# Kernel optimization log

Measured on AMD Instinct MI355X. Metric: run time of the kernel, lower is better.

## Reference

```python
import jax, jax.numpy as jnp
import numpy as np

N, E, D, H, O = 50000, 800000, 128, 256, 64
BN_EPS = 1e-5


def setup_inputs() -> dict:
    key = jax.random.key(0)
    ks = jax.random.split(key, 12)
    x_indices = jnp.arange(N, dtype=jnp.int64) if jax.config.jax_enable_x64 else jnp.arange(N, dtype=jnp.int32)
    ei = jax.random.randint(ks[0], (2, E), 0, N, dtype=jnp.int32)
    s = lambda k, shape, fan: jax.random.normal(k, shape, dtype=jnp.float32) * (1.0 / np.sqrt(fan))
    return {
        "x_indices": x_indices,
        "ei": ei,
        "emb": jax.random.normal(ks[1], (N, D), dtype=jnp.float32),
        "W1": s(ks[2], (D, H), D), "b1": jnp.zeros((H,), jnp.float32),
        "g1": jnp.ones((H,), jnp.float32), "be1": jnp.zeros((H,), jnp.float32),
        "W2": s(ks[3], (H, H), H), "b2": jnp.zeros((H,), jnp.float32),
        "g2": jnp.ones((H,), jnp.float32), "be2": jnp.zeros((H,), jnp.float32),
        "W3": s(ks[4], (H, O), H), "b3": jnp.zeros((O,), jnp.float32),
    }


def reference(x_indices, ei, emb, W1, b1, g1, be1, W2, b2, g2, be2, W3, b3):
    n = emb.shape[0]
    # GCN normalization with self-loops (PyG GCNConv default):
    loop = jnp.arange(n, dtype=ei.dtype)
    row = jnp.concatenate([ei[0], loop])  # source
    col = jnp.concatenate([ei[1], loop])  # target (aggregation index)
    deg = jax.ops.segment_sum(jnp.ones_like(col, dtype=emb.dtype), col, num_segments=n)
    dinv = jnp.where(deg > 0, 1.0 / jnp.sqrt(jnp.maximum(deg, 1.0)), 0.0)
    norm = dinv[row] * dinv[col]  # [E+N]

    def conv(x, W, b):
        xl = x @ W                                   # [N, d_out]
        msg = xl[row] * norm[:, None]                # gather + scale
        return jax.ops.segment_sum(msg, col, num_segments=n) + b  # scatter-add

    def bn(x, g, be):  # batch-stat BatchNorm1d (training-mode stats)
        m = jnp.mean(x, axis=0)
        v = jnp.var(x, axis=0)
        return (x - m) * (g / jnp.sqrt(v + BN_EPS)) + be

    x = emb[x_indices]
    x = jax.nn.relu(bn(conv(x, W1, b1), g1, be1))
    x = jax.nn.relu(bn(conv(x, W2, b2), g2, be2))
    return conv(x, W3, b3)
```

## Files before the change

kernel.cpp:

```cpp
#include <hip/hip_runtime.h>
#include <hip/hip_bf16.h>

#define Dk 128
#define Hk 256
#define Ok 64
#define BN_EPS 1e-5f

typedef __attribute__((ext_vector_type(8))) short short8;
typedef __attribute__((ext_vector_type(4))) float f32x4;

static __device__ __forceinline__ float bf2f(ushort u) {
    union { uint32_t i; float f; } c; c.i = ((uint32_t)u) << 16; return c.f;
}
static __device__ __forceinline__ ushort f2bf(float f) {
    union { float f; uint32_t u; } c; c.f = f;
    return (ushort)((c.u + 0x7fffu + ((c.u >> 16) & 1u)) >> 16);
}

template<int V> __device__ __forceinline__ void loadv(ushort* d, const ushort* s);
template<> __device__ __forceinline__ void loadv<1>(ushort* d, const ushort* s) { d[0] = *s; }
template<> __device__ __forceinline__ void loadv<2>(ushort* d, const ushort* s) { *(ushort2*)d = *(const ushort2*)s; }
template<> __device__ __forceinline__ void loadv<4>(ushort* d, const ushort* s) { *(ushort4*)d = *(const ushort4*)s; }
template<int V> __device__ __forceinline__ void storev(ushort* d, const ushort* s);
template<> __device__ __forceinline__ void storev<1>(ushort* d, const ushort* s) { *d = s[0]; }
template<> __device__ __forceinline__ void storev<2>(ushort* d, const ushort* s) { *(ushort2*)d = *(const ushort2*)s; }
template<> __device__ __forceinline__ void storev<4>(ushort* d, const ushort* s) { *(ushort4*)d = *(const ushort4*)s; }


__global__ void count_kernel(const int* __restrict__ col, int* __restrict__ cnt, int E) {
    int e = blockIdx.x * blockDim.x + threadIdx.x;
    if (e < E) atomicAdd(&cnt[col[e]], 1);
}

__global__ void dinv_bsum_kernel(const int* __restrict__ cnt, float* __restrict__ dinv,
                                 int* __restrict__ fillc, int* __restrict__ bsum, int n) {
    __shared__ int sm[256];
    int i = blockIdx.x * 256 + threadIdx.x;
    int c = (i < n) ? cnt[i] : 0;
    if (i < n) { dinv[i] = rsqrtf((float)c + 1.0f); fillc[i] = 0; }
    sm[threadIdx.x] = c;
    __syncthreads();
    for (int s = 128; s; s >>= 1) {
        if (threadIdx.x < s) sm[threadIdx.x] += sm[threadIdx.x + s];
        __syncthreads();
    }
    if (!threadIdx.x) bsum[blockIdx.x] = sm[0];
}

__global__ void scan_base_kernel(int* __restrict__ bsum, int nb) {
    __shared__ int sm[256];
    int t = threadIdx.x;
    int carry = 0;
    for (int base = 0; base < nb; base += 256) {
        int i = base + t;
        int v = (i < nb) ? bsum[i] : 0;
        sm[t] = v;
        __syncthreads();
        for (int s = 1; s < 256; s <<= 1) {
            int add = (t >= s) ? sm[t - s] : 0;
            __syncthreads();
            sm[t] += add;
            __syncthreads();
        }
        if (i < nb) bsum[i] = carry + sm[t] - v;
        int tot = sm[255];
        __syncthreads();
        carry += tot;
    }
}

__global__ void scan_final_kernel(const int* __restrict__ cnt, const int* __restrict__ bbase,
                                  int* __restrict__ offv, int n) {
    __shared__ int sm[256];
    int t = threadIdx.x, i = blockIdx.x * 256 + t;
    int v = (i < n) ? cnt[i] : 0;
    sm[t] = v;
    __syncthreads();
    for (int s = 1; s < 256; s <<= 1) {
        int add = (t >= s) ? sm[t - s] : 0;
        __syncthreads();
        sm[t] += add;
        __syncthreads();
    }
    if (i < n) offv[i + 1] = bbase[blockIdx.x] + sm[t];
    if (i == 0) offv[0] = 0;
}

__global__ void fill_kernel(const int* __restrict__ row, const int* __restrict__ col,
                            const int* __restrict__ off, int* __restrict__ fillc,
                            const float* __restrict__ dinv, int2* __restrict__ ep, int E) {
    int e = blockIdx.x * blockDim.x + threadIdx.x;
    if (e < E) {
        int c = col[e], r = row[e];
        int p = atomicAdd(&fillc[c], 1);
        ep[off[c] + p] = make_int2(r, __float_as_int(dinv[r]));
    }
}


__global__ void emb_cvt_kernel(const float* __restrict__ emb, const int* __restrict__ xidx,
                               ushort* __restrict__ out, int n) {
    int gid = blockIdx.x * 256 + threadIdx.x;
    int total = n * (Dk / 8);
    if (gid >= total) return;
    int node = gid >> 4, seg = gid & 15;
    int src = xidx[node];
    const float* p = &emb[(size_t)src * Dk + seg * 8];
    float4 lo = *(const float4*)p, hi = *(const float4*)(p + 4);
    ushort r[8] = {f2bf(lo.x), f2bf(lo.y), f2bf(lo.z), f2bf(lo.w),
                   f2bf(hi.x), f2bf(hi.y), f2bf(hi.z), f2bf(hi.w)};
    *(short8*)&out[(size_t)gid * 8] = *(short8*)r;
}

#define W1SZ (Dk * Hk)
#define W2SZ (Hk * Hk)
#define W3SZ (Hk * Ok)
__global__ void wcvt_all_kernel(const float* __restrict__ W1, const float* __restrict__ W2,
                                const float* __restrict__ W3, ushort* __restrict__ W1t,
                                ushort* __restrict__ W2t, ushort* __restrict__ W3t,
                                float* __restrict__ stats) {
    int gid = blockIdx.x * 256 + threadIdx.x;
    if (blockIdx.x == (W1SZ + W2SZ + W3SZ) / 256) {
        for (int i = threadIdx.x; i < 1024; i += 256) stats[i] = 0.f;
        return;
    }
    if (gid < W1SZ) {
        int c = gid / Dk, k = gid - c * Dk;
        W1t[gid] = f2bf(W1[(size_t)k * Hk + c]);
    } else if (gid < W1SZ + W2SZ) {
        int idx = gid - W1SZ;
        int c = idx / Hk, k = idx - c * Hk;
        W2t[idx] = f2bf(W2[(size_t)k * Hk + c]);
    } else {
        int idx = gid - W1SZ - W2SZ;
        int c = idx / Hk, k = idx - c * Hk;
        W3t[idx] = f2bf(W3[(size_t)k * Ok + c]);
    }
}


template<int KD, int BNT, bool STATS, bool BIAS, bool BN_A>
__global__ __launch_bounds__(256) void gemm128(
    const ushort* __restrict__ A, const ushort* __restrict__ Wt,
    ushort* __restrict__ Cout, int n, int Hout,
    const float* __restrict__ bias, float* __restrict__ stats,
    const float* __restrict__ statsIn, const float* __restrict__ g,
    const float* __restrict__ be, float invn)
{
    constexpr int WN = (BNT == 128) ? 2 : 1;
    constexpr int MR = (BNT == 128) ? 4 : 2;
    constexpr int NR = 4;
    __shared__ ushort lds[(128 + BNT) * 32];
    __shared__ float ssc[BN_A ? KD : 1];
    __shared__ float ssh[BN_A ? KD : 1];
    ushort* As = lds;
    ushort* Bs = lds + 128 * 32;

    const int tid = threadIdx.x;
    const int lane = tid & 63, wid = tid >> 6;
    const int wr = wid / WN, wc = wid % WN;
    const int lr = lane & 15, lg = lane >> 4;
    const int bm = blockIdx.x * 128;
    const int bn = blockIdx.y * BNT;

    if (BN_A) {
        for (int f = tid; f < KD; f += 256) {
            float mean = statsIn[f] * invn;
            float var = statsIn[KD + f] * invn - mean * mean;
            float sc = g[f] * rsqrtf(var + BN_EPS);
            ssc[f] = sc;
            ssh[f] = fmaf(-mean, sc, be[f]);
        }
        __syncthreads();
    }

    f32x4 acc[MR][NR] = {};

    for (int k0 = 0; k0 < KD; k0 += 32) {
        #pragma unroll
        for (int c = 0; c < 2; ++c) {
            int boff = wid * 2048 + c * 1024 + lane * 16;
            int row = boff >> 6;
            int k8 = (boff >> 4) & 3;
            int grow = bm + row; if (grow >= n) grow = n - 1;
            const ushort* src = &A[(size_t)grow * KD + k0 + k8 * 8];
            if (BN_A) {
                short8 av = *(const short8*)src;
                ushort r[8];
                #pragma unroll
                for (int j = 0; j < 8; ++j) {
                    int kf = k0 + k8 * 8 + j;
                    float v = bf2f((ushort)av[j]);
                    r[j] = f2bf(fmaxf(fmaf(v, ssc[kf], ssh[kf]), 0.f));
                }
                *(short8*)&As[row * 32 + k8 * 8] = *(short8*)r;
            } else {
                __builtin_amdgcn_global_load_lds(
                    (const __attribute__((address_space(1))) void*)src,
                    (__attribute__((address_space(3))) void*)&As[(wid * 2048 + c * 1024) >> 1],
                    16, 0, 0);
            }
        }
        constexpr int BC = BNT * 64 / 4096;
        #pragma unroll
        for (int c = 0; c < BC; ++c) {
            int boff = wid * (BNT * 16) + c * 1024 + lane * 16;
            int col = boff >> 6;
            int k8 = (boff >> 4) & 3;
            const ushort* src = &Wt[(size_t)(bn + col) * KD + k0 + k8 * 8];
            __builtin_amdgcn_global_load_lds(
                (const __attribute__((address_space(1))) void*)src,
                (__attribute__((address_space(3))) void*)&Bs[(wid * (BNT * 16) + c * 1024) >> 1],
                16, 0, 0);
        }
        __syncthreads();

        short8 af[MR], bfr[NR];
        #pragma unroll
        for (int m = 0; m < MR; ++m)
            af[m] = *(const short8*)&As[(wr * MR * 16 + m * 16 + lr) * 32 + lg * 8];
        #pragma unroll
        for (int nn = 0; nn < NR; ++nn)
            bfr[nn] = *(const short8*)&Bs[(wc * NR * 16 + nn * 16 + lr) * 32 + lg * 8];
        #pragma unroll
        for (int m = 0; m < MR; ++m)
            #pragma unroll
            for (int nn = 0; nn < NR; ++nn)
                acc[m][nn] = __builtin_amdgcn_mfma_f32_16x16x32_bf16(af[m], bfr[nn], acc[m][nn], 0, 0, 0);
        __syncthreads();
    }

    float s[NR], q[NR];
    #pragma unroll
    for (int nn = 0; nn < NR; ++nn) { s[nn] = 0.f; q[nn] = 0.f; }
    #pragma unroll
    for (int nn = 0; nn < NR; ++nn) {
        int col = bn + wc * NR * 16 + nn * 16 + lr;
        float bv = BIAS ? bias[col] : 0.f;
        #pragma unroll
        for (int m = 0; m < MR; ++m) {
            #pragma unroll
            for (int i = 0; i < 4; ++i) {
                int row = bm + wr * MR * 16 + m * 16 + lg * 4 + i;
                if (row < n) {
                    float v = acc[m][nn][i] + bv;
                    Cout[(size_t)row * Hout + col] = f2bf(v);
                    if (STATS) { s[nn] += v; q[nn] += v * v; }
                }
            }
        }
    }
    if (STATS) {
        #pragma unroll
        for (int nn = 0; nn < NR; ++nn) {
            s[nn] += __shfl_xor(s[nn], 16);
            q[nn] += __shfl_xor(q[nn], 16);
            s[nn] += __shfl_xor(s[nn], 32);
            q[nn] += __shfl_xor(q[nn], 32);
            if (lg == 0) {
                int col = bn + wc * NR * 16 + nn * 16 + lr;
                atomicAdd(&stats[col], s[nn]);
                atomicAdd(&stats[Hout + col], q[nn]);
            }
        }
    }
}


template<int FH, int MODE>
__global__ __launch_bounds__(256) void agg_kernel(
    const ushort* __restrict__ x, const int2* __restrict__ ep, const int* __restrict__ off,
    const float* __restrict__ dinv, const float* __restrict__ statsIn,
    const float* __restrict__ g, const float* __restrict__ be, float invn,
    const float* __restrict__ bias, void* __restrict__ outp, int n)
{
    constexpr int VEC = FH / 64;
    const int lane = threadIdx.x & 63;
    const int wid = __builtin_amdgcn_readfirstlane(threadIdx.x >> 6);
    const int node = blockIdx.x * 4 + wid;
    if (node >= n) return;
    const int fb = lane * VEC;
    const ushort* __restrict__ xb = x + fb;

    float sc[VEC], sh[VEC];
    if (MODE == 1) {
        #pragma unroll
        for (int v = 0; v < VEC; ++v) {
            int f = fb + v;
            float mean = statsIn[f] * invn;
            float var = statsIn[FH + f] * invn - mean * mean;
            sc[v] = g[f] * rsqrtf(var + BN_EPS);
            sh[v] = fmaf(-mean, sc[v], be[f]);
        }
    }
    auto xform = [&](ushort u, int v) -> float {
        float val = bf2f(u);
        if (MODE == 1) val = fmaxf(fmaf(val, sc[v], sh[v]), 0.f);
        return val;
    };

    float di = dinv[node];
    float acc[VEC];
    {
        ushort t[VEC];
        loadv<VEC>(t, &xb[(size_t)node * FH]);
        #pragma unroll
        for (int v = 0; v < VEC; ++v) acc[v] = di * xform(t[v], v);
    }
    const int e1 = off[node + 1];
    int e = off[node];
    for (; e + 8 <= e1; e += 8) {
        int2 p[8];
        ushort t[8][VEC];
        #pragma unroll
        for (int j = 0; j < 8; ++j) p[j] = ep[e + j];
        #pragma unroll
        for (int j = 0; j < 8; ++j) loadv<VEC>(t[j], &xb[(size_t)p[j].x * FH]);
        #pragma unroll
        for (int j = 0; j < 8; ++j) {
            float w = __int_as_float(p[j].y);
            #pragma unroll
            for (int v = 0; v < VEC; ++v) acc[v] = fmaf(w, xform(t[j][v], v), acc[v]);
        }
    }
    for (; e + 2 <= e1; e += 2) {
        int2 p0 = ep[e], p1 = ep[e + 1];
        ushort t0[VEC], t1[VEC];
        loadv<VEC>(t0, &xb[(size_t)p0.x * FH]);
        loadv<VEC>(t1, &xb[(size_t)p1.x * FH]);
        float w0 = __int_as_float(p0.y), w1 = __int_as_float(p1.y);
        #pragma unroll
        for (int v = 0; v < VEC; ++v) {
            acc[v] = fmaf(w0, xform(t0[v], v), acc[v]);
            acc[v] = fmaf(w1, xform(t1[v], v), acc[v]);
        }
    }
    if (e < e1) {
        int2 pp = ep[e];
        ushort tt[VEC];
        loadv<VEC>(tt, &xb[(size_t)pp.x * FH]);
        float w = __int_as_float(pp.y);
        #pragma unroll
        for (int v = 0; v < VEC; ++v) acc[v] = fmaf(w, xform(tt[v], v), acc[v]);
    }
    if (MODE == 2) {
        float* o = (float*)outp + (size_t)node * FH + fb;
        #pragma unroll
        for (int v = 0; v < VEC; ++v) o[v] = fmaf(di, acc[v], bias[fb + v]);
    } else {
        ushort ov[VEC];
        #pragma unroll
        for (int v = 0; v < VEC; ++v) ov[v] = f2bf(di * acc[v]);
        storev<VEC>((ushort*)outp + (size_t)node * FH + fb, ov);
    }
}


extern "C" void kernel_launch(void* const* d_in, const int* in_sizes, int n_in,
                              void* d_out, int out_size, void* d_ws, size_t ws_size,
                              hipStream_t stream) {
    const int*   x_idx = (const int*)d_in[0];
    const int*   ei    = (const int*)d_in[1];
    const float* emb   = (const float*)d_in[2];
    const float* W1    = (const float*)d_in[3];
    const float* b1    = (const float*)d_in[4];
    const float* g1    = (const float*)d_in[5];
    const float* be1   = (const float*)d_in[6];
    const float* W2    = (const float*)d_in[7];
    const float* b2    = (const float*)d_in[8];
    const float* g2    = (const float*)d_in[9];
    const float* be2   = (const float*)d_in[10];
    const float* W3    = (const float*)d_in[11];
    const float* b3    = (const float*)d_in[12];

    const int N = in_sizes[0];
    const int E = in_sizes[1] / 2;
    const int* erow = ei;
    const int* ecol = ei + E;

    char* p = (char*)d_ws;
    auto alloc = [&](size_t bytes) { char* q = p; p += (bytes + 255) & ~(size_t)255; return q; };
    const int nb = (N + 255) / 256;
    float*  dinv  = (float*) alloc((size_t)N * 4);
    int*    cnt   = (int*)   alloc((size_t)N * 4);
    int*    off   = (int*)   alloc((size_t)(N + 1) * 4);
    int*    fillc = (int*)   alloc((size_t)N * 4);
    int*    bsum  = (int*)   alloc((size_t)nb * 4);
    int2*   ep    = (int2*)  alloc((size_t)E * 8);
    float*  stats = (float*) alloc(1024 * 4);
    float*  stats1 = stats, *stats2 = stats + 512;
    ushort* W1t   = (ushort*)alloc((size_t)Dk * Hk * 2);
    ushort* W2t   = (ushort*)alloc((size_t)Hk * Hk * 2);
    ushort* W3t   = (ushort*)alloc((size_t)Hk * Ok * 2);
    ushort* bufU  = (ushort*)alloc((size_t)N * Hk * 2);
    ushort* embb  = bufU;
    ushort* agg1b = bufU + (size_t)N * Dk;
    ushort* conv2b= bufU;
    ushort* conv1b= (ushort*)alloc((size_t)N * Hk * 2);
    ushort* agg2b = (ushort*)alloc((size_t)N * Hk * 2);
    ushort* xl3b  = (ushort*)alloc((size_t)N * Ok * 2);

    const float invn = 1.0f / (float)N;

    hipMemsetAsync(cnt, 0, (size_t)N * 4, stream);
    count_kernel<<<(E + 255) / 256, 256, 0, stream>>>(ecol, cnt, E);
    dinv_bsum_kernel<<<nb, 256, 0, stream>>>(cnt, dinv, fillc, bsum, N);
    scan_base_kernel<<<1, 256, 0, stream>>>(bsum, nb);
    scan_final_kernel<<<nb, 256, 0, stream>>>(cnt, bsum, off, N);
    fill_kernel<<<(E + 255) / 256, 256, 0, stream>>>(erow, ecol, off, fillc, dinv, ep, E);

    emb_cvt_kernel<<<(N * (Dk / 8) + 255) / 256, 256, 0, stream>>>(emb, x_idx, embb, N);
    wcvt_all_kernel<<<(W1SZ + W2SZ + W3SZ) / 256 + 1, 256, 0, stream>>>(
        W1, W2, W3, W1t, W2t, W3t, stats);

    const int rb128 = (N + 127) / 128;
    const int aggBlocks = (N + 3) / 4;

    agg_kernel<Dk, 0><<<aggBlocks, 256, 0, stream>>>(
        embb, ep, off, dinv, nullptr, nullptr, nullptr, 0.f, nullptr, agg1b, N);
    gemm128<Dk, 128, true, true, false><<<dim3(rb128, Hk / 128), 256, 0, stream>>>(
        agg1b, W1t, conv1b, N, Hk, b1, stats1, nullptr, nullptr, nullptr, 0.f);

    agg_kernel<Hk, 1><<<aggBlocks, 256, 0, stream>>>(
        conv1b, ep, off, dinv, stats1, g1, be1, invn, nullptr, agg2b, N);
    gemm128<Hk, 128, true, true, false><<<dim3(rb128, Hk / 128), 256, 0, stream>>>(
        agg2b, W2t, conv2b, N, Hk, b2, stats2, nullptr, nullptr, nullptr, 0.f);

    gemm128<Hk, 64, false, false, true><<<dim3(rb128, 1), 256, 0, stream>>>(
        conv2b, W3t, xl3b, N, Ok, nullptr, nullptr, stats2, g2, be2, invn);
    agg_kernel<Ok, 2><<<aggBlocks, 256, 0, stream>>>(
        xl3b, ep, off, dinv, nullptr, nullptr, nullptr, 0.f, b3, d_out, N);
}
```

Before: 323.2 us.

## Double-buffer GEMM LDS tiles, shard BN stat atomics, add BN finalize kernel

```diff
diff --git a/kernel.cpp b/kernel.cpp
--- a/kernel.cpp
+++ b/kernel.cpp
@@ -115,15 +115,20 @@
 #define W1SZ (Dk * Hk)
 #define W2SZ (Hk * Hk)
 #define W3SZ (Hk * Ok)
+#define WBLK ((W1SZ + W2SZ + W3SZ) / 256)
+#define STATSP_FLOATS (2 * 64 * 512)
 __global__ void wcvt_all_kernel(const float* __restrict__ W1, const float* __restrict__ W2,
                                 const float* __restrict__ W3, ushort* __restrict__ W1t,
                                 ushort* __restrict__ W2t, ushort* __restrict__ W3t,
-                                float* __restrict__ stats) {
-    int gid = blockIdx.x * 256 + threadIdx.x;
-    if (blockIdx.x == (W1SZ + W2SZ + W3SZ) / 256) {
-        for (int i = threadIdx.x; i < 1024; i += 256) stats[i] = 0.f;
+                                float* __restrict__ statsP) {
+    int bid = blockIdx.x;
+    if (bid >= WBLK) {
+        int idx = (bid - WBLK) * 1024 + threadIdx.x * 4;
+        if (idx < STATSP_FLOATS)
+            *(float4*)&statsP[idx] = make_float4(0.f, 0.f, 0.f, 0.f);
         return;
     }
+    int gid = bid * 256 + threadIdx.x;
     if (gid < W1SZ) {
         int c = gid / Dk, k = gid - c * Dk;
         W1t[gid] = f2bf(W1[(size_t)k * Hk + c]);
@@ -138,23 +143,38 @@
     }
 }
 
+__global__ void bn_finalize_kernel(const float* __restrict__ statsP, const float* __restrict__ g,
+                                   const float* __restrict__ be, float* __restrict__ ss,
+                                   float invn) {
+    int f = threadIdx.x;
+    float sum = 0.f, sq = 0.f;
+    for (int s = 0; s < 64; ++s) {
+        sum += statsP[s * 512 + f];
+        sq  += statsP[s * 512 + 256 + f];
+    }
+    float mean = sum * invn;
+    float var = sq * invn - mean * mean;
+    float sc = g[f] * rsqrtf(var + BN_EPS);
+    ss[f] = sc;
+    ss[256 + f] = fmaf(-mean, sc, be[f]);
+}
+
 
 template<int KD, int BNT, bool STATS, bool BIAS, bool BN_A>
 __global__ __launch_bounds__(256) void gemm128(
     const ushort* __restrict__ A, const ushort* __restrict__ Wt,
     ushort* __restrict__ Cout, int n, int Hout,
-    const float* __restrict__ bias, float* __restrict__ stats,
-    const float* __restrict__ statsIn, const float* __restrict__ g,
-    const float* __restrict__ be, float invn)
+    const float* __restrict__ bias, float* __restrict__ statsP,
+    const float* __restrict__ ss)
 {
     constexpr int WN = (BNT == 128) ? 2 : 1;
     constexpr int MR = (BNT == 128) ? 4 : 2;
     constexpr int NR = 4;
-    __shared__ ushort lds[(128 + BNT) * 32];
+    constexpr int TILE = (128 + BNT) * 32;
+    constexpr int NT = KD / 32;
+    __shared__ ushort lds[2 * TILE];
     __shared__ float ssc[BN_A ? KD : 1];
     __shared__ float ssh[BN_A ? KD : 1];
-    ushort* As = lds;
-    ushort* Bs = lds + 128 * 32;
 
     const int tid = threadIdx.x;
     const int lane = tid & 63, wid = tid >> 6;
@@ -165,18 +185,15 @@
 
     if (BN_A) {
         for (int f = tid; f < KD; f += 256) {
-            float mean = statsIn[f] * invn;
-            float var = statsIn[KD + f] * invn - mean * mean;
-            float sc = g[f] * rsqrtf(var + BN_EPS);
-            ssc[f] = sc;
-            ssh[f] = fmaf(-mean, sc, be[f]);
-        }
-        __syncthreads();
-    }
-
-    f32x4 acc[MR][NR] = {};
-
-    for (int k0 = 0; k0 < KD; k0 += 32) {
+            ssc[f] = ss[f];
+            ssh[f] = ss[KD + f];
+        }
+        __syncthreads();
+    }
+
+    auto stage = [&](int buf, int k0) {
+        ushort* As = lds + buf * TILE;
+        ushort* Bs = As + 128 * 32;
         #pragma unroll
         for (int c = 0; c < 2; ++c) {
             int boff = wid * 2048 + c * 1024 + lane * 16;
@@ -213,8 +230,17 @@
                 (__attribute__((address_space(3))) void*)&Bs[(wid * (BNT * 16) + c * 1024) >> 1],
                 16, 0, 0);
         }
-        __syncthreads();
-
+    };
+
+    f32x4 acc[MR][NR] = {};
+
+    stage(0, 0);
+    __syncthreads();
+    int cur = 0;
+    for (int t = 0; t < NT; ++t) {
+        if (t + 1 < NT) stage(cur ^ 1, (t + 1) * 32);
+        ushort* As = lds + cur * TILE;
+        ushort* Bs = As + 128 * 32;
         short8 af[MR], bfr[NR];
         #pragma unroll
         for (int m = 0; m < MR; ++m)
@@ -228,6 +254,7 @@
             for (int nn = 0; nn < NR; ++nn)
                 acc[m][nn] = __builtin_amdgcn_mfma_f32_16x16x32_bf16(af[m], bfr[nn], acc[m][nn], 0, 0, 0);
         __syncthreads();
+        cur ^= 1;
     }
 
     float s[NR], q[NR];
@@ -251,6 +278,7 @@
         }
     }
     if (STATS) {
+        float* sp = statsP + (size_t)(blockIdx.x & 63) * 512;
         #pragma unroll
         for (int nn = 0; nn < NR; ++nn) {
             s[nn] += __shfl_xor(s[nn], 16);
@@ -259,8 +287,8 @@
             q[nn] += __shfl_xor(q[nn], 32);
             if (lg == 0) {
                 int col = bn + wc * NR * 16 + nn * 16 + lr;
-                atomicAdd(&stats[col], s[nn]);
-                atomicAdd(&stats[Hout + col], q[nn]);
+                atomicAdd(&sp[col], s[nn]);
+                atomicAdd(&sp[256 + col], q[nn]);
             }
         }
     }
@@ -270,8 +298,7 @@
 template<int FH, int MODE>
 __global__ __launch_bounds__(256) void agg_kernel(
     const ushort* __restrict__ x, const int2* __restrict__ ep, const int* __restrict__ off,
-    const float* __restrict__ dinv, const float* __restrict__ statsIn,
-    const float* __restrict__ g, const float* __restrict__ be, float invn,
+    const float* __restrict__ dinv, const float* __restrict__ ss,
     const float* __restrict__ bias, void* __restrict__ outp, int n)
 {
     constexpr int VEC = FH / 64;
@@ -285,13 +312,7 @@
     float sc[VEC], sh[VEC];
     if (MODE == 1) {
         #pragma unroll
-        for (int v = 0; v < VEC; ++v) {
-            int f = fb + v;
-            float mean = statsIn[f] * invn;
-            float var = statsIn[FH + f] * invn - mean * mean;
-            sc[v] = g[f] * rsqrtf(var + BN_EPS);
-            sh[v] = fmaf(-mean, sc[v], be[f]);
-        }
+        for (int v = 0; v < VEC; ++v) { sc[v] = ss[fb + v]; sh[v] = ss[FH + fb + v]; }
     }
     auto xform = [&](ushort u, int v) -> float {
         float val = bf2f(u);
@@ -387,8 +408,10 @@
     int*    fillc = (int*)   alloc((size_t)N * 4);
     int*    bsum  = (int*)   alloc((size_t)nb * 4);
     int2*   ep    = (int2*)  alloc((size_t)E * 8);
-    float*  stats = (float*) alloc(1024 * 4);
-    float*  stats1 = stats, *stats2 = stats + 512;
+    float*  statsP= (float*) alloc((size_t)STATSP_FLOATS * 4);
+    float*  stats1P = statsP, *stats2P = statsP + 64 * 512;
+    float*  ss1   = (float*) alloc(512 * 4);
+    float*  ss2   = (float*) alloc(512 * 4);
     ushort* W1t   = (ushort*)alloc((size_t)Dk * Hk * 2);
     ushort* W2t   = (ushort*)alloc((size_t)Hk * Hk * 2);
     ushort* W3t   = (ushort*)alloc((size_t)Hk * Ok * 2);
@@ -410,24 +433,26 @@
     fill_kernel<<<(E + 255) / 256, 256, 0, stream>>>(erow, ecol, off, fillc, dinv, ep, E);
 
     emb_cvt_kernel<<<(N * (Dk / 8) + 255) / 256, 256, 0, stream>>>(emb, x_idx, embb, N);
-    wcvt_all_kernel<<<(W1SZ + W2SZ + W3SZ) / 256 + 1, 256, 0, stream>>>(
-        W1, W2, W3, W1t, W2t, W3t, stats);
+    wcvt_all_kernel<<<WBLK + (STATSP_FLOATS + 1023) / 1024, 256, 0, stream>>>(
+        W1, W2, W3, W1t, W2t, W3t, statsP);
 
     const int rb128 = (N + 127) / 128;
     const int aggBlocks = (N + 3) / 4;
 
     agg_kernel<Dk, 0><<<aggBlocks, 256, 0, stream>>>(
-        embb, ep, off, dinv, nullptr, nullptr, nullptr, 0.f, nullptr, agg1b, N);
+        embb, ep, off, dinv, nullptr, nullptr, agg1b, N);
     gemm128<Dk, 128, true, true, false><<<dim3(rb128, Hk / 128), 256, 0, stream>>>(
-        agg1b, W1t, conv1b, N, Hk, b1, stats1, nullptr, nullptr, nullptr, 0.f);
+        agg1b, W1t, conv1b, N, Hk, b1, stats1P, nullptr);
+    bn_finalize_kernel<<<1, 256, 0, stream>>>(stats1P, g1, be1, ss1, invn);
 
     agg_kernel<Hk, 1><<<aggBlocks, 256, 0, stream>>>(
-        conv1b, ep, off, dinv, stats1, g1, be1, invn, nullptr, agg2b, N);
+        conv1b, ep, off, dinv, ss1, nullptr, agg2b, N);
     gemm128<Hk, 128, true, true, false><<<dim3(rb128, Hk / 128), 256, 0, stream>>>(
-        agg2b, W2t, conv2b, N, Hk, b2, stats2, nullptr, nullptr, nullptr, 0.f);
+        agg2b, W2t, conv2b, N, Hk, b2, stats2P, nullptr);
+    bn_finalize_kernel<<<1, 256, 0, stream>>>(stats2P, g2, be2, ss2, invn);
 
     gemm128<Hk, 64, false, false, true><<<dim3(rb128, 1), 256, 0, stream>>>(
-        conv2b, W3t, xl3b, N, Ok, nullptr, nullptr, stats2, g2, be2, invn);
+        conv2b, W3t, xl3b, N, Ok, nullptr, nullptr, ss2);
     agg_kernel<Ok, 2><<<aggBlocks, 256, 0, stream>>>(
-        xl3b, ep, off, dinv, nullptr, nullptr, nullptr, 0.f, b3, d_out, N);
-}
+        xl3b, ep, off, dinv, nullptr, b3, d_out, N);
+}
```

Result: faster. 284.4 us (-12.0%).
